# Kernel optimization log

Measured on AMD Instinct MI355X. Metric: run time of the kernel, lower is better.

The kernel has to match this reference:

```python
import jax, jax.numpy as jnp
import numpy as np


def setup_inputs() -> dict:
    key = jax.random.key(0)
    k1, k2, k3, k4, k5 = jax.random.split(key, 5)
    B, S, T = 512, 1024, 32
    emissions = jax.random.normal(k1, (B, S, T), dtype=jnp.float32)
    tags = jax.random.randint(k2, (B, S), 0, T, dtype=jnp.int64)
    mask = jnp.ones((B, S), dtype=jnp.float32)  # all positions valid; mask[:,0]==1 required
    transitions = jax.random.normal(k3, (T, T), dtype=jnp.float32)
    start_transitions = jax.random.normal(k4, (T,), dtype=jnp.float32)
    end_transitions = jax.random.normal(k5, (T,), dtype=jnp.float32)
    return {
        "emissions": emissions,
        "tags": tags,
        "mask": mask,
        "transitions": transitions,
        "start_transitions": start_transitions,
        "end_transitions": end_transitions,
    }


def _compute_score(emissions, tags, mask, transitions, start_transitions, end_transitions):
    # score of the gold path, fully vectorized over time
    # first step
    score = start_transitions[tags[:, 0]]
    score = score + jnp.take_along_axis(emissions[:, 0], tags[:, 0:1], axis=1)[:, 0]
    # steps 1..S-1
    emit = jnp.take_along_axis(emissions[:, 1:], tags[:, 1:, None], axis=2)[..., 0]  # [B,S-1]
    trans = transitions[tags[:, :-1], tags[:, 1:]]                                   # [B,S-1]
    score = score + ((emit + trans) * mask[:, 1:]).sum(axis=1)
    # end transition from the last valid tag
    last_idx = mask.sum(axis=1).astype(jnp.int32) - 1                                # [B]
    last_tags = jnp.take_along_axis(tags, last_idx[:, None].astype(tags.dtype), axis=1)[:, 0]
    score = score + end_transitions[last_tags]
    return score


def _compute_partition(emissions, mask, transitions, start_transitions, end_transitions):
    # forward algorithm: logsumexp scan over time
    alpha0 = start_transitions + emissions[:, 0]  # [B,T]

    def step(alpha, inp):
        e_i, m_i = inp  # e_i: [B,T], m_i: [B]
        # alpha[b,i] + transitions[i,j] + e_i[b,j] -> logsumexp over i
        scores = alpha[:, :, None] + transitions[None, :, :] + e_i[:, None, :]  # [B,T,T]
        next_alpha = jax.nn.logsumexp(scores, axis=1)                            # [B,T]
        m = m_i[:, None]
        alpha = next_alpha * m + alpha * (1.0 - m)
        return alpha, None

    xs = (jnp.swapaxes(emissions[:, 1:], 0, 1), jnp.swapaxes(mask[:, 1:], 0, 1))
    alpha, _ = jax.lax.scan(step, alpha0, xs)
    alpha = alpha + end_transitions
    return jax.nn.logsumexp(alpha, axis=1)  # [B]


def reference(emissions, tags, mask, transitions, start_transitions, end_transitions):
    score = _compute_score(emissions, tags, mask, transitions, start_transitions, end_transitions)
    partition = _compute_partition(emissions, mask, transitions, start_transitions, end_transitions)
    return -(score - partition).sum()
```

## Files before the change

kernel.cpp:

```cpp
#include <hip/hip_runtime.h>


typedef __attribute__((ext_vector_type(8)))  short    short8;
typedef __attribute__((ext_vector_type(16))) float    f32x16;
typedef __attribute__((ext_vector_type(4)))  unsigned uint4v;

#define S_N 1024
#define T_N 32
#define B_N 512
#define L_CH 64
#define C_CH 16
#define SCALE_MUL 0.0078125f
#define SCALE_LOG 4.852030263919617f

#define WS_FRAG_DW ((size_t)B_N * C_CH * 512)
#define WS_MSUM_OFF (WS_FRAG_DW)
#define WS_SCORE_OFF (WS_FRAG_DW + 512)
#define WS_NAPP_OFF (WS_FRAG_DW + 1024)

#if __has_builtin(__builtin_amdgcn_cvt_pk_bf16_f32)
typedef __attribute__((ext_vector_type(2))) __bf16 bf16x2;
__device__ __forceinline__ unsigned cvtpk(float lo, float hi) {
    return __builtin_bit_cast(unsigned, __builtin_amdgcn_cvt_pk_bf16_f32(lo, hi));
}
#else
__device__ __forceinline__ unsigned cvtpk(float lo, float hi) {
    const unsigned a = __float_as_uint(lo) + 0x8000u;
    const unsigned b = __float_as_uint(hi) + 0x8000u;
    return __builtin_amdgcn_perm(b, a, 0x07060302u);
}
#endif

__device__ __forceinline__ short8 mk8(const unsigned* a) {
    uint4v u = {a[0], a[1], a[2], a[3]};
    return __builtin_bit_cast(short8, u);
}
__device__ __forceinline__ float bflo(unsigned u) { return __uint_as_float(u << 16); }
__device__ __forceinline__ float bfhi(unsigned u) { return __uint_as_float(u & 0xFFFF0000u); }
__device__ __forceinline__ int PIx(int x) { return (x & ~12) | ((x & 4) << 1) | ((x & 8) >> 1); }

__global__ __launch_bounds__(256, 2) void crf_chunk(
    const float* __restrict__ em, const int* __restrict__ tags,
    const float* __restrict__ mask, const float* __restrict__ trans,
    const float* __restrict__ startT, unsigned* __restrict__ wsf,
    float* __restrict__ wsflt)
{
    __shared__ unsigned elds[16384];
    const int wib  = threadIdx.x >> 6;
    const int lane = threadIdx.x & 63;
    const int n    = lane & 31;
    const int h    = lane >> 5;
    const int b    = blockIdx.x;

    #pragma unroll
    for (int q = 0; q < 4; ++q) {
        const float* eq = em + ((size_t)b * S_N + (4 * wib + q) * L_CH) * T_N;
        unsigned* mq = elds + wib * 4096 + q * 1024;
        #pragma unroll
        for (int i = 0; i < 16; ++i) {
            const int flat = i * 64 + lane;
            const int r = flat >> 4, m = flat & 15;
            const int base = ((m & 4) << 2) + ((m & 2) << 2) + ((m & 1) << 1) + ((m >> 3) << 2);
            const float2 v = *(const float2*)(eq + r * 32 + base);
            mq[r * 16 + m] = cvtpk(__expf(v.x) * SCALE_MUL, __expf(v.y) * SCALE_MUL);
        }
    }

    unsigned long long mb_[4];
    {
        float vacc = 0.f, macc = 0.f;
        #pragma unroll
        for (int q = 0; q < 4; ++q) {
            const int c = 4 * wib + q;
            const int s = c * L_CH + lane;
            const float mv = mask[b * S_N + s];
            unsigned long long mb = __ballot(mv != 0.0f);
            if (c == 0) mb &= ~1ull;
            mb_[q] = mb;
            const int tc = tags[b * S_N + s];
            int tp = __shfl_up(tc, 1, 64);
            float val;
            if (lane == 0) {
                if (c == 0) {
                    val = startT[tc] + em[(size_t)b * S_N * T_N + tc];
                } else {
                    tp = tags[b * S_N + s - 1];
                    val = mv * (em[((size_t)b * S_N + s) * T_N + tc] + trans[tp * 32 + tc]);
                }
            } else {
                val = mv * (em[((size_t)b * S_N + s) * T_N + tc] + trans[tp * 32 + tc]);
            }
            vacc += val; macc += mv;
            if (lane == 0) wsflt[WS_NAPP_OFF + b * C_CH + c] = (float)__popcll(mb);
        }
        #pragma unroll
        for (int d = 32; d > 0; d >>= 1) {
            vacc += __shfl_xor(vacc, d, 64);
            macc += __shfl_xor(macc, d, 64);
        }
        if (lane == 0) {
            atomicAdd(&wsflt[WS_SCORE_OFF + b], vacc);
            atomicAdd(&wsflt[WS_MSUM_OFF + b], macc);
        }
    }

    unsigned A1[4], A2[4];
    #pragma unroll
    for (int j = 0; j < 4; ++j) {
        const int k1 = PIx(8 * h + 2 * j);
        const int k2 = PIx(16 + 8 * h + 2 * j);
        A1[j] = cvtpk(__expf(trans[n * 32 + k1]), __expf(trans[n * 32 + k1 + 1]));
        A2[j] = cvtpk(__expf(trans[n * 32 + k2]), __expf(trans[n * 32 + k2 + 1]));
    }
    const short8 A1v = mk8(A1), A2v = mk8(A2);
    const f32x16 Zacc = {};

    f32x16 D0, D1, D2, D3;
    #pragma unroll
    for (int i = 0; i < 16; ++i) {
        const int row = (i & 3) + 8 * (i >> 2) + 4 * h;
        const float v = (row == n) ? 1.0f : 0.0f;
        D0[i] = v; D1[i] = v; D2[i] = v; D3[i] = v;
    }

    const unsigned* m0 = elds + wib * 4096;
    const unsigned* m1 = m0 + 1024;
    const unsigned* m2 = m0 + 2048;
    const unsigned* m3 = m0 + 3072;

    #define STEP(D, mq, r_) { \
        const uint4 su = *(const uint4*)((mq) + (r_) * 16 + h * 8); \
        const uint4 sv = *(const uint4*)((mq) + (r_) * 16 + h * 8 + 4); \
        unsigned S[8]; \
        S[0] = cvtpk(D[0]  * bflo(su.x), D[1]  * bfhi(su.x)); \
        S[1] = cvtpk(D[2]  * bflo(su.y), D[3]  * bfhi(su.y)); \
        S[2] = cvtpk(D[4]  * bflo(su.z), D[5]  * bfhi(su.z)); \
        S[3] = cvtpk(D[6]  * bflo(su.w), D[7]  * bfhi(su.w)); \
        S[4] = cvtpk(D[8]  * bflo(sv.x), D[9]  * bfhi(sv.x)); \
        S[5] = cvtpk(D[10] * bflo(sv.y), D[11] * bfhi(sv.y)); \
        S[6] = cvtpk(D[12] * bflo(sv.z), D[13] * bfhi(sv.z)); \
        S[7] = cvtpk(D[14] * bflo(sv.w), D[15] * bfhi(sv.w)); \
        f32x16 t_ = __builtin_amdgcn_mfma_f32_32x32x16_bf16(A1v, mk8(&S[0]), Zacc, 0, 0, 0); \
        D = __builtin_amdgcn_mfma_f32_32x32x16_bf16(A2v, mk8(&S[4]), t_, 0, 0, 0); \
    }

    const bool allclean =
        ((mb_[0] | ((4 * wib) == 0 ? 1ull : 0ull)) == ~0ull) &&
        (mb_[1] == ~0ull) && (mb_[2] == ~0ull) && (mb_[3] == ~0ull);

    if (allclean) {
        #pragma unroll 2
        for (int r = L_CH - 1; r >= 1; --r) {
            STEP(D0, m0, r); STEP(D1, m1, r); STEP(D2, m2, r); STEP(D3, m3, r);
        }
        if (mb_[0] & 1ull) STEP(D0, m0, 0);
        if (mb_[1] & 1ull) STEP(D1, m1, 0);
        if (mb_[2] & 1ull) STEP(D2, m2, 0);
        if (mb_[3] & 1ull) STEP(D3, m3, 0);
    } else {
        for (int r = L_CH - 1; r >= 0; --r) {
            if ((mb_[0] >> r) & 1ull) STEP(D0, m0, r);
            if ((mb_[1] >> r) & 1ull) STEP(D1, m1, r);
            if ((mb_[2] >> r) & 1ull) STEP(D2, m2, r);
            if ((mb_[3] >> r) & 1ull) STEP(D3, m3, r);
        }
    }
    #undef STEP

    #define STORE(D, q_) { \
        unsigned* dst = wsf + ((size_t)(b * C_CH + 4 * wib + (q_)) * 64 + lane) * 8; \
        ((uint4*)dst)[0] = make_uint4(cvtpk(D[0], D[1]),   cvtpk(D[2], D[3]), \
                                      cvtpk(D[4], D[5]),   cvtpk(D[6], D[7])); \
        ((uint4*)dst)[1] = make_uint4(cvtpk(D[8], D[9]),   cvtpk(D[10], D[11]), \
                                      cvtpk(D[12], D[13]), cvtpk(D[14], D[15])); \
    }
    STORE(D0, 0) STORE(D1, 1) STORE(D2, 2) STORE(D3, 3)
    #undef STORE
}

__global__ __launch_bounds__(256) void crf_combine(
    const float* __restrict__ em, const int* __restrict__ tags,
    const float* __restrict__ startT, const float* __restrict__ endT,
    const unsigned* __restrict__ wsf, const float* __restrict__ wsflt,
    float* __restrict__ out)
{
    const int lane = threadIdx.x & 63;
    const int n = lane & 31, h = lane >> 5;
    const int b = blockIdx.x * 4 + (threadIdx.x >> 6);

    int idxA[8], idxB[8];
    #pragma unroll
    for (int j = 0; j < 8; ++j) {
        idxA[j] = PIx(8 * h + j);
        idxB[j] = PIx(16 + 8 * h + j);
    }

    float a0 = startT[n] + em[(size_t)b * S_N * T_N + n];
    float m = a0;
    #pragma unroll
    for (int d = 16; d > 0; d >>= 1) m = fmaxf(m, __shfl_xor(m, d, 32));
    float A = __expf(a0 - m);
    float Lacc = m;
    float ntot = (lane < 16) ? wsflt[WS_NAPP_OFF + b * C_CH + lane] : 0.0f;

    const uint4* fb = (const uint4*)(wsf + (size_t)b * C_CH * 512);
    uint4 q0 = fb[lane * 2];
    uint4 q1 = fb[lane * 2 + 1];

    for (int c = 0; c < C_CH; ++c) {
        uint4 n0 = q0, n1 = q1;
        if (c + 1 < C_CH) {
            n0 = fb[(c + 1) * 128 + lane * 2];
            n1 = fb[(c + 1) * 128 + lane * 2 + 1];
        }

        float p0 = 0.f, p1 = 0.f, p2 = 0.f, p3 = 0.f;
        p0 = fmaf(__shfl(A, idxA[0], 32), bflo(q0.x), p0);
        p1 = fmaf(__shfl(A, idxA[1], 32), bfhi(q0.x), p1);
        p2 = fmaf(__shfl(A, idxA[2], 32), bflo(q0.y), p2);
        p3 = fmaf(__shfl(A, idxA[3], 32), bfhi(q0.y), p3);
        p0 = fmaf(__shfl(A, idxA[4], 32), bflo(q0.z), p0);
        p1 = fmaf(__shfl(A, idxA[5], 32), bfhi(q0.z), p1);
        p2 = fmaf(__shfl(A, idxA[6], 32), bflo(q0.w), p2);
        p3 = fmaf(__shfl(A, idxA[7], 32), bfhi(q0.w), p3);
        p0 = fmaf(__shfl(A, idxB[0], 32), bflo(q1.x), p0);
        p1 = fmaf(__shfl(A, idxB[1], 32), bfhi(q1.x), p1);
        p2 = fmaf(__shfl(A, idxB[2], 32), bflo(q1.y), p2);
        p3 = fmaf(__shfl(A, idxB[3], 32), bfhi(q1.y), p3);
        p0 = fmaf(__shfl(A, idxB[4], 32), bflo(q1.z), p0);
        p1 = fmaf(__shfl(A, idxB[5], 32), bfhi(q1.z), p1);
        p2 = fmaf(__shfl(A, idxB[6], 32), bflo(q1.w), p2);
        p3 = fmaf(__shfl(A, idxB[7], 32), bfhi(q1.w), p3);
        float part = (p0 + p1) + (p2 + p3);
        part += __shfl_xor(part, 32);

        float mm = part;
        #pragma unroll
        for (int d = 16; d > 0; d >>= 1) mm = fmaxf(mm, __shfl_xor(mm, d, 32));
        A = part / mm;
        Lacc += __logf(mm);
        q0 = n0; q1 = n1;
    }

    float v = A * __expf(endT[n]);
    #pragma unroll
    for (int d = 16; d > 0; d >>= 1) {
        v    += __shfl_xor(v, d, 32);
        ntot += __shfl_xor(ntot, d, 32);
    }
    if (lane == 0) {
        const int len = (int)(wsflt[WS_MSUM_OFF + b] + 0.5f);
        const int lt  = tags[b * S_N + len - 1];
        const float res = Lacc + __logf(v) + ntot * SCALE_LOG
                          - endT[lt] - wsflt[WS_SCORE_OFF + b];
        atomicAdd(out, res);
    }
}

extern "C" void kernel_launch(void* const* d_in, const int* in_sizes, int n_in,
                              void* d_out, int out_size, void* d_ws, size_t ws_size,
                              hipStream_t stream) {
    const float* em     = (const float*)d_in[0];
    const int*   tags   = (const int*)  d_in[1];
    const float* mask   = (const float*)d_in[2];
    const float* trans  = (const float*)d_in[3];
    const float* startT = (const float*)d_in[4];
    const float* endT   = (const float*)d_in[5];
    float* out = (float*)d_out;

    unsigned* wsf   = (unsigned*)d_ws;
    float*    wsflt = (float*)d_ws;

    hipMemsetAsync(out, 0, sizeof(float), stream);
    hipMemsetAsync((char*)d_ws + WS_MSUM_OFF * 4, 0, 4096, stream);

    hipLaunchKernelGGL(crf_chunk, dim3(512), dim3(256), 0, stream,
                       em, tags, mask, trans, startT, wsf, wsflt);
    hipLaunchKernelGGL(crf_combine, dim3(128), dim3(256), 0, stream,
                       em, tags, startT, endT, wsf, wsflt, out);
}
```

Measured before the change: 173.2 us.

## Halve chunk length, double chunk grid, precompute transition fragments in prep kernel

Splits each sequence into 32 chunks of 32 steps instead of 16 of 64, launching two blocks per batch element with smaller LDS and higher occupancy bounds. The exp(transition) bf16 MFMA operand is built once by a tiny prep kernel and loaded from workspace instead of recomputed per wave. This shortens the serial MFMA chain per wave and increases parallelism, at the cost of doubling the sequential chunk combinations in the combine kernel and adding an extra launch.

```diff
diff --git a/kernel.cpp b/kernel.cpp
--- a/kernel.cpp
+++ b/kernel.cpp
@@ -8,15 +8,16 @@
 #define S_N 1024
 #define T_N 32
 #define B_N 512
-#define L_CH 64
-#define C_CH 16
+#define L_CH 32
+#define C_CH 32
 #define SCALE_MUL 0.0078125f
 #define SCALE_LOG 4.852030263919617f
 
 #define WS_FRAG_DW ((size_t)B_N * C_CH * 512)
 #define WS_MSUM_OFF (WS_FRAG_DW)
 #define WS_SCORE_OFF (WS_FRAG_DW + 512)
-#define WS_NAPP_OFF (WS_FRAG_DW + 1024)
+#define WS_A_OFF (WS_FRAG_DW + 1024)
+#define WS_NAPP_OFF (WS_FRAG_DW + 1536)
 
 #if __has_builtin(__builtin_amdgcn_cvt_pk_bf16_f32)
 typedef __attribute__((ext_vector_type(2))) __bf16 bf16x2;
@@ -39,25 +40,45 @@
 __device__ __forceinline__ float bfhi(unsigned u) { return __uint_as_float(u & 0xFFFF0000u); }
 __device__ __forceinline__ int PIx(int x) { return (x & ~12) | ((x & 4) << 1) | ((x & 8) >> 1); }
 
-__global__ __launch_bounds__(256, 2) void crf_chunk(
+__global__ __launch_bounds__(64) void crf_prep(
+    const float* __restrict__ trans, unsigned* __restrict__ wsf)
+{
+    const int lane = threadIdx.x;
+    const int n = lane & 31, h = lane >> 5;
+    unsigned A1[4], A2[4];
+    #pragma unroll
+    for (int j = 0; j < 4; ++j) {
+        const int k1 = PIx(8 * h + 2 * j);
+        const int k2 = PIx(16 + 8 * h + 2 * j);
+        A1[j] = cvtpk(__expf(trans[n * 32 + k1]), __expf(trans[n * 32 + k1 + 1]));
+        A2[j] = cvtpk(__expf(trans[n * 32 + k2]), __expf(trans[n * 32 + k2 + 1]));
+    }
+    unsigned* dst = wsf + WS_A_OFF + lane * 8;
+    ((uint4*)dst)[0] = make_uint4(A1[0], A1[1], A1[2], A1[3]);
+    ((uint4*)dst)[1] = make_uint4(A2[0], A2[1], A2[2], A2[3]);
+}
+
+__global__ __launch_bounds__(256, 4) void crf_chunk(
     const float* __restrict__ em, const int* __restrict__ tags,
     const float* __restrict__ mask, const float* __restrict__ trans,
     const float* __restrict__ startT, unsigned* __restrict__ wsf,
     float* __restrict__ wsflt)
 {
-    __shared__ unsigned elds[16384];
+    __shared__ unsigned elds[16][512];
     const int wib  = threadIdx.x >> 6;
     const int lane = threadIdx.x & 63;
     const int n    = lane & 31;
     const int h    = lane >> 5;
-    const int b    = blockIdx.x;
+    const int b    = blockIdx.x >> 1;
+    const int half = blockIdx.x & 1;
+    const int c0   = half * 16 + wib * 4;
 
     #pragma unroll
     for (int q = 0; q < 4; ++q) {
-        const float* eq = em + ((size_t)b * S_N + (4 * wib + q) * L_CH) * T_N;
-        unsigned* mq = elds + wib * 4096 + q * 1024;
+        const float* eq = em + ((size_t)b * S_N + (c0 + q) * L_CH) * T_N;
+        unsigned* mq = elds[wib * 4 + q];
         #pragma unroll
-        for (int i = 0; i < 16; ++i) {
+        for (int i = 0; i < 8; ++i) {
             const int flat = i * 64 + lane;
             const int r = flat >> 4, m = flat & 15;
             const int base = ((m & 4) << 2) + ((m & 2) << 2) + ((m & 1) << 1) + ((m >> 3) << 2);
@@ -66,22 +87,21 @@
         }
     }
 
-    unsigned long long mb_[4];
+    unsigned mb_[4];
     {
         float vacc = 0.f, macc = 0.f;
         #pragma unroll
-        for (int q = 0; q < 4; ++q) {
-            const int c = 4 * wib + q;
-            const int s = c * L_CH + lane;
+        for (int q2 = 0; q2 < 2; ++q2) {
+            const int s  = c0 * L_CH + q2 * 64 + lane;
             const float mv = mask[b * S_N + s];
-            unsigned long long mb = __ballot(mv != 0.0f);
-            if (c == 0) mb &= ~1ull;
-            mb_[q] = mb;
+            const unsigned long long mb = __ballot(mv != 0.0f);
+            mb_[2 * q2]     = (unsigned)mb;
+            mb_[2 * q2 + 1] = (unsigned)(mb >> 32);
             const int tc = tags[b * S_N + s];
             int tp = __shfl_up(tc, 1, 64);
             float val;
             if (lane == 0) {
-                if (c == 0) {
+                if (s == 0) {
                     val = startT[tc] + em[(size_t)b * S_N * T_N + tc];
                 } else {
                     tp = tags[b * S_N + s - 1];
@@ -91,8 +111,8 @@
                 val = mv * (em[((size_t)b * S_N + s) * T_N + tc] + trans[tp * 32 + tc]);
             }
             vacc += val; macc += mv;
-            if (lane == 0) wsflt[WS_NAPP_OFF + b * C_CH + c] = (float)__popcll(mb);
-        }
+        }
+        if (c0 == 0) mb_[0] &= ~1u;
         #pragma unroll
         for (int d = 32; d > 0; d >>= 1) {
             vacc += __shfl_xor(vacc, d, 64);
@@ -101,18 +121,16 @@
         if (lane == 0) {
             atomicAdd(&wsflt[WS_SCORE_OFF + b], vacc);
             atomicAdd(&wsflt[WS_MSUM_OFF + b], macc);
-        }
-    }
-
-    unsigned A1[4], A2[4];
-    #pragma unroll
-    for (int j = 0; j < 4; ++j) {
-        const int k1 = PIx(8 * h + 2 * j);
-        const int k2 = PIx(16 + 8 * h + 2 * j);
-        A1[j] = cvtpk(__expf(trans[n * 32 + k1]), __expf(trans[n * 32 + k1 + 1]));
-        A2[j] = cvtpk(__expf(trans[n * 32 + k2]), __expf(trans[n * 32 + k2 + 1]));
-    }
-    const short8 A1v = mk8(A1), A2v = mk8(A2);
+            #pragma unroll
+            for (int q = 0; q < 4; ++q)
+                wsflt[WS_NAPP_OFF + b * C_CH + c0 + q] = (float)__popc(mb_[q]);
+        }
+    }
+
+    const uint4 ua = ((const uint4*)(wsf + WS_A_OFF))[lane * 2];
+    const uint4 ub = ((const uint4*)(wsf + WS_A_OFF))[lane * 2 + 1];
+    const short8 A1v = mk8((const unsigned*)&ua);
+    const short8 A2v = mk8((const unsigned*)&ub);
     const f32x16 Zacc = {};
 
     f32x16 D0, D1, D2, D3;
@@ -123,10 +141,10 @@
         D0[i] = v; D1[i] = v; D2[i] = v; D3[i] = v;
     }
 
-    const unsigned* m0 = elds + wib * 4096;
-    const unsigned* m1 = m0 + 1024;
-    const unsigned* m2 = m0 + 2048;
-    const unsigned* m3 = m0 + 3072;
+    const unsigned* m0 = elds[wib * 4];
+    const unsigned* m1 = elds[wib * 4 + 1];
+    const unsigned* m2 = elds[wib * 4 + 2];
+    const unsigned* m3 = elds[wib * 4 + 3];
 
     #define STEP(D, mq, r_) { \
         const uint4 su = *(const uint4*)((mq) + (r_) * 16 + h * 8); \
@@ -145,30 +163,30 @@
     }
 
     const bool allclean =
-        ((mb_[0] | ((4 * wib) == 0 ? 1ull : 0ull)) == ~0ull) &&
-        (mb_[1] == ~0ull) && (mb_[2] == ~0ull) && (mb_[3] == ~0ull);
+        ((mb_[0] | (c0 == 0 ? 1u : 0u)) == 0xFFFFFFFFu) &&
+        (mb_[1] == 0xFFFFFFFFu) && (mb_[2] == 0xFFFFFFFFu) && (mb_[3] == 0xFFFFFFFFu);
 
     if (allclean) {
         #pragma unroll 2
         for (int r = L_CH - 1; r >= 1; --r) {
             STEP(D0, m0, r); STEP(D1, m1, r); STEP(D2, m2, r); STEP(D3, m3, r);
         }
-        if (mb_[0] & 1ull) STEP(D0, m0, 0);
-        if (mb_[1] & 1ull) STEP(D1, m1, 0);
-        if (mb_[2] & 1ull) STEP(D2, m2, 0);
-        if (mb_[3] & 1ull) STEP(D3, m3, 0);
+        if (mb_[0] & 1u) STEP(D0, m0, 0);
+        if (mb_[1] & 1u) STEP(D1, m1, 0);
+        if (mb_[2] & 1u) STEP(D2, m2, 0);
+        if (mb_[3] & 1u) STEP(D3, m3, 0);
     } else {
         for (int r = L_CH - 1; r >= 0; --r) {
-            if ((mb_[0] >> r) & 1ull) STEP(D0, m0, r);
-            if ((mb_[1] >> r) & 1ull) STEP(D1, m1, r);
-            if ((mb_[2] >> r) & 1ull) STEP(D2, m2, r);
-            if ((mb_[3] >> r) & 1ull) STEP(D3, m3, r);
+            if ((mb_[0] >> r) & 1u) STEP(D0, m0, r);
+            if ((mb_[1] >> r) & 1u) STEP(D1, m1, r);
+            if ((mb_[2] >> r) & 1u) STEP(D2, m2, r);
+            if ((mb_[3] >> r) & 1u) STEP(D3, m3, r);
         }
     }
     #undef STEP
 
     #define STORE(D, q_) { \
-        unsigned* dst = wsf + ((size_t)(b * C_CH + 4 * wib + (q_)) * 64 + lane) * 8; \
+        unsigned* dst = wsf + ((size_t)(b * C_CH + c0 + (q_)) * 64 + lane) * 8; \
         ((uint4*)dst)[0] = make_uint4(cvtpk(D[0], D[1]),   cvtpk(D[2], D[3]), \
                                       cvtpk(D[4], D[5]),   cvtpk(D[6], D[7])); \
         ((uint4*)dst)[1] = make_uint4(cvtpk(D[8], D[9]),   cvtpk(D[10], D[11]), \
@@ -201,7 +219,7 @@
     for (int d = 16; d > 0; d >>= 1) m = fmaxf(m, __shfl_xor(m, d, 32));
     float A = __expf(a0 - m);
     float Lacc = m;
-    float ntot = (lane < 16) ? wsflt[WS_NAPP_OFF + b * C_CH + lane] : 0.0f;
+    float ntot = (lane < 32) ? wsflt[WS_NAPP_OFF + b * C_CH + lane] : 0.0f;
 
     const uint4* fb = (const uint4*)(wsf + (size_t)b * C_CH * 512);
     uint4 q0 = fb[lane * 2];
@@ -274,7 +292,8 @@
     hipMemsetAsync(out, 0, sizeof(float), stream);
     hipMemsetAsync((char*)d_ws + WS_MSUM_OFF * 4, 0, 4096, stream);
 
-    hipLaunchKernelGGL(crf_chunk, dim3(512), dim3(256), 0, stream,
+    hipLaunchKernelGGL(crf_prep, dim3(1), dim3(64), 0, stream, trans, wsf);
+    hipLaunchKernelGGL(crf_chunk, dim3(1024), dim3(256), 0, stream,
                        em, tags, mask, trans, startT, wsf, wsflt);
     hipLaunchKernelGGL(crf_combine, dim3(128), dim3(256), 0, stream,
                        em, tags, startT, endT, wsf, wsflt, out);
```

Result: slower. 179.5 us (+3.6%).
